# Kernel tuning notes

Hardware: AMD Instinct MI355X
Metric: run time of the kernel (lower is better)

The kernel has to match this reference:

```python
import jax, jax.numpy as jnp
import numpy as np

EMBED_DIM = 1024
NUM_HEADS = 16
HEAD_DIM = EMBED_DIM // NUM_HEADS


def setup_inputs() -> dict:
    key = jax.random.key(0)
    k_x, k_qkv, k_w, k_b = jax.random.split(key, 4)
    B, N, C = 2, 2048, EMBED_DIM
    scale = 1.0 / np.sqrt(C)
    x = jax.random.normal(k_x, (B, N, C), dtype=jnp.float32)
    # nn.Linear(embed_dim, 3*embed_dim, bias=False): weight [3C, C]
    w_qkv = jax.random.normal(k_qkv, (3 * C, C), dtype=jnp.float32) * scale
    # nn.Linear(embed_dim, embed_dim): weight [C, C], bias [C]
    w_out = jax.random.normal(k_w, (C, C), dtype=jnp.float32) * scale
    b_out = jax.random.normal(k_b, (C,), dtype=jnp.float32) * scale
    return {"x": x, "w_qkv": w_qkv, "w_out": w_out, "b_out": b_out}


def reference(x, w_qkv, w_out, b_out):
    B, N, C = x.shape
    H, D = NUM_HEADS, HEAD_DIM
    # qkv projection: [B,N,3C] -> [3,B,H,N,D]
    qkv = jnp.einsum("bnc,fc->bnf", x, w_qkv)
    qkv = qkv.reshape(B, N, 3, H, D).transpose(2, 0, 3, 1, 4)
    q, k, v = qkv[0], qkv[1], qkv[2]
    # scaled dot-product attention (dropout p=0 / eval mode -> identity)
    scores = jnp.einsum("bhnd,bhmd->bhnm", q, k) / np.sqrt(D).astype(x.dtype)
    attn = jax.nn.softmax(scores, axis=-1)
    out = jnp.einsum("bhnm,bhmd->bhnd", attn, v)
    out = out.transpose(0, 2, 1, 3).reshape(B, N, C)
    return jnp.einsum("bnc,oc->bno", out, w_out) + b_out
```

## Files before the change

### kernel.cpp

```cpp
#include <hip/hip_runtime.h>
#include <hip/hip_bf16.h>

typedef unsigned short u16;
typedef __attribute__((ext_vector_type(4))) float f32x4;
typedef __attribute__((ext_vector_type(8))) short bf16x8;

#define MFMA16(a, b, c) __builtin_amdgcn_mfma_f32_16x16x32_bf16(a, b, c, 0, 0, 0)

__device__ __forceinline__ u16 f2bf(float f) {
    union { float f; unsigned u; } v;
    v.f = f;
    unsigned r = v.u + 0x7FFFu + ((v.u >> 16) & 1u);
    return (u16)(r >> 16);
}

__device__ __forceinline__ float bf2f(u16 h) {
    union { unsigned u; float f; } v;
    v.u = ((unsigned)h) << 16;
    return v.f;
}

__device__ __forceinline__ int4 pack8(const float4 a, const float4 b) {
    int4 r;
    r.x = (int)((unsigned)f2bf(a.x) | ((unsigned)f2bf(a.y) << 16));
    r.y = (int)((unsigned)f2bf(a.z) | ((unsigned)f2bf(a.w) << 16));
    r.z = (int)((unsigned)f2bf(b.x) | ((unsigned)f2bf(b.y) << 16));
    r.w = (int)((unsigned)f2bf(b.z) | ((unsigned)f2bf(b.w) << 16));
    return r;
}

__device__ __forceinline__ unsigned pk2(float a, float b) {
    __hip_bfloat162 t = __float22bfloat162_rn(make_float2(a, b));
    union { __hip_bfloat162 h; unsigned u; } c;
    c.h = t;
    return c.u;
}

__device__ __forceinline__ bf16x8 mk_pa(f32x4 a, f32x4 b) {
    union { uint4 u; bf16x8 v; } r;
    r.u.x = pk2(a[0], a[1]);
    r.u.y = pk2(a[2], a[3]);
    r.u.z = pk2(b[0], b[1]);
    r.u.w = pk2(b[2], b[3]);
    return r.v;
}

__device__ __forceinline__ void gload_lds16(const u16* g, u16* l) {
    __builtin_amdgcn_global_load_lds(
        (const __attribute__((address_space(1))) void*)g,
        (__attribute__((address_space(3))) void*)l, 16, 0, 0);
}

__global__ __launch_bounds__(256) void cvt_kernel(
    const float* __restrict__ x, const float* __restrict__ wq,
    const float* __restrict__ wo, u16* __restrict__ outb)
{
    size_t i = ((size_t)blockIdx.x * 256 + threadIdx.x) * 8;
    const float* src;
    size_t off;
    if (i < 4194304)      { src = x;  off = i; }
    else if (i < 7340032) { src = wq; off = i - 4194304; }
    else                  { src = wo; off = i - 7340032; }
    float4 a = *(const float4*)(src + off);
    float4 b = *(const float4*)(src + off + 4);
    *(int4*)(outb + i) = pack8(a, b);
}

__global__ __launch_bounds__(512) void qkv_gemm_kernel(
    const u16* __restrict__ X, const u16* __restrict__ W,
    u16* __restrict__ qws, u16* __restrict__ kws, u16* __restrict__ vws)
{
    __shared__ __align__(16) u16 Ash[256 * 64];
    __shared__ __align__(16) u16 Bsh[128 * 64];
    const int id = blockIdx.x;
    const int xcd = id & 7, slot = id >> 3;
    const int bm = (xcd >> 1) * 4 + (slot & 3);
    const int bn = (xcd & 1) * 12 + (slot >> 2);
    const int tid = threadIdx.x;
    const int lane = tid & 63, wid = tid >> 6;
    const int wm = wid >> 1, wn = wid & 1;
    const int g = lane >> 4, lq = lane & 15;

    f32x4 acc[4][4];
#pragma unroll
    for (int i = 0; i < 4; i++)
#pragma unroll
        for (int j = 0; j < 4; j++) acc[i][j] = (f32x4){0.f, 0.f, 0.f, 0.f};

    const int lrow = lane >> 3;
    const int lchunk = (lane & 7) ^ lrow;
    const u16* Ab = X + (size_t)(bm * 256 + lrow) * 1024 + lchunk * 8;
    const u16* Bb = W + (size_t)(bn * 128 + lrow) * 1024 + lchunk * 8;

    for (int kt = 0; kt < 16; ++kt) {
#pragma unroll
        for (int i = 0; i < 4; i++) {
            int sub = wid * 4 + i;
            gload_lds16(Ab + (size_t)sub * 8192 + kt * 64, &Ash[sub * 512]);
        }
#pragma unroll
        for (int i = 0; i < 2; i++) {
            int sub = wid * 2 + i;
            gload_lds16(Bb + (size_t)sub * 8192 + kt * 64, &Bsh[sub * 512]);
        }
        __syncthreads();
#pragma unroll
        for (int ka = 0; ka < 2; ka++) {
            bf16x8 af[4], bfr[4];
#pragma unroll
            for (int mt = 0; mt < 4; mt++) {
                int row = wm * 64 + mt * 16 + lq;
                af[mt] = *(const bf16x8*)&Ash[row * 64 + (((ka * 4 + g) ^ (row & 7)) << 3)];
            }
#pragma unroll
            for (int nt = 0; nt < 4; nt++) {
                int row = wn * 64 + nt * 16 + lq;
                bfr[nt] = *(const bf16x8*)&Bsh[row * 64 + (((ka * 4 + g) ^ (row & 7)) << 3)];
            }
#pragma unroll
            for (int mt = 0; mt < 4; mt++)
#pragma unroll
                for (int nt = 0; nt < 4; nt++)
                    acc[mt][nt] = MFMA16(af[mt], bfr[nt], acc[mt][nt]);
        }
        __syncthreads();
    }

#pragma unroll
    for (int mt = 0; mt < 4; mt++) {
#pragma unroll
        for (int nt = 0; nt < 4; nt++) {
            int f = bn * 128 + wn * 64 + nt * 16 + lq;
            int t = f >> 10, h = (f >> 6) & 15, d = f & 63;
            int mbase = bm * 256 + wm * 64 + mt * 16 + g * 4;
            int b = mbase >> 11, n0 = mbase & 2047;
            if (t == 0) {
#pragma unroll
                for (int r = 0; r < 4; r++)
                    qws[((size_t)(b * 16 + h) * 2048 + n0 + r) * 64 + d] =
                        f2bf(acc[mt][nt][r] * 0.18033688f);
            } else if (t == 1) {
#pragma unroll
                for (int r = 0; r < 4; r++)
                    kws[((size_t)(b * 16 + h) * 2048 + n0 + r) * 64 + d] =
                        f2bf(acc[mt][nt][r]);
            } else {
                ushort4 pk;
                pk.x = f2bf(acc[mt][nt][0]);
                pk.y = f2bf(acc[mt][nt][1]);
                pk.z = f2bf(acc[mt][nt][2]);
                pk.w = f2bf(acc[mt][nt][3]);
                *(ushort4*)&vws[((size_t)(b * 16 + h) * 64 + d) * 2048 + n0] = pk;
            }
        }
    }
}

__global__ __launch_bounds__(256, 2) void attn_kernel(
    const u16* __restrict__ qws, const u16* __restrict__ kws,
    const u16* __restrict__ vws, u16* __restrict__ Opart,
    float* __restrict__ lpart)
{
    __shared__ __align__(16) u16 Ksh[2][64 * 64];
    __shared__ __align__(16) u16 Vsh[2][64 * 64];
    const int bh = blockIdx.x, qt = blockIdx.y, kvh = blockIdx.z;
    const int tid = threadIdx.x, wid = tid >> 6, lane = tid & 63;
    const int g = lane >> 4, lq = lane & 15;

    const u16* Qp = qws + ((size_t)bh * 2048 + qt * 128 + wid * 32) * 64;
    bf16x8 qf[2][2];
#pragma unroll
    for (int qa = 0; qa < 2; qa++) {
        qf[qa][0] = *(const bf16x8*)(Qp + (qa * 16 + lq) * 64 + g * 8);
        qf[qa][1] = *(const bf16x8*)(Qp + (qa * 16 + lq) * 64 + 32 + g * 8);
    }

    const int lr8 = lane >> 3;
    const int c0 = ((lane & 7) - lr8) & 7;
    const u16* Kb = kws + (size_t)bh * 2048 * 64;
    const u16* Vb = vws + (size_t)bh * 64 * 2048;

#define STAGE(TG, BUF)                                                        \
    {                                                                         \
        _Pragma("unroll")                                                     \
        for (int i = 0; i < 2; i++) {                                         \
            int sub = wid * 2 + i;                                            \
            int c = (c0 - 2 * sub) & 7;                                       \
            gload_lds16(Kb + (size_t)((TG) * 64 + sub * 8 + lr8) * 64 + c * 8,\
                        &Ksh[BUF][sub * 512]);                                \
            gload_lds16(Vb + (size_t)(sub * 8 + lr8) * 2048 + (TG) * 64 + c * 8,\
                        &Vsh[BUF][sub * 512]);                                \
        }                                                                     \
    }

    int koff[4][2];
#pragma unroll
    for (int j = 0; j < 4; j++) {
        int R = (j >> 1) * 32 + (lq >> 2) * 8 + (j & 1) * 4 + (lq & 3);
        koff[j][0] = R * 64 + (((g)     + (R & 7) + 2 * (R >> 3)) & 7) * 8;
        koff[j][1] = R * 64 + (((4 + g) + (R & 7) + 2 * (R >> 3)) & 7) * 8;
    }
    int voff[4][2];
#pragma unroll
    for (int dt = 0; dt < 4; dt++) {
        int vr = dt * 16 + lq;
        voff[dt][0] = vr * 64 + (((g)     + (vr & 7) + 2 * (vr >> 3)) & 7) * 8;
        voff[dt][1] = vr * 64 + (((4 + g) + (vr & 7) + 2 * (vr >> 3)) & 7) * 8;
    }

    bf16x8 onesB;
#pragma unroll
    for (int i = 0; i < 8; i++) onesB[i] = (short)0x3F80;

    f32x4 oacc[2][4];
#pragma unroll
    for (int qa = 0; qa < 2; qa++)
#pragma unroll
        for (int i = 0; i < 4; i++) oacc[qa][i] = (f32x4){0.f, 0.f, 0.f, 0.f};
    f32x4 lacc[2];
#pragma unroll
    for (int qa = 0; qa < 2; qa++) lacc[qa] = (f32x4){0.f, 0.f, 0.f, 0.f};

    const int tbase = kvh * 16;
    STAGE(tbase + 0, 0);

    for (int t = 0; t < 16; ++t) {
        const int buf = t & 1;
        asm volatile("s_waitcnt vmcnt(0)" ::: "memory");
        __builtin_amdgcn_s_barrier();
        __builtin_amdgcn_sched_barrier(0);
        if (t < 15) STAGE(tbase + t + 1, buf ^ 1);

        const u16* Kt = Ksh[buf];
        const u16* Vt = Vsh[buf];

        bf16x8 pa0[2], pa1[2];
        {
            f32x4 za[2], zb[2];
            bf16x8 k0 = *(const bf16x8*)&Kt[koff[0][0]];
            bf16x8 k1 = *(const bf16x8*)&Kt[koff[0][1]];
#pragma unroll
            for (int qa = 0; qa < 2; qa++) {
                f32x4 z = (f32x4){0.f, 0.f, 0.f, 0.f};
                z = MFMA16(k0, qf[qa][0], z);
                z = MFMA16(k1, qf[qa][1], z);
                za[qa] = z;
            }
            k0 = *(const bf16x8*)&Kt[koff[1][0]];
            k1 = *(const bf16x8*)&Kt[koff[1][1]];
#pragma unroll
            for (int qa = 0; qa < 2; qa++) {
                f32x4 z = (f32x4){0.f, 0.f, 0.f, 0.f};
                z = MFMA16(k0, qf[qa][0], z);
                z = MFMA16(k1, qf[qa][1], z);
                zb[qa] = z;
            }
#pragma unroll
            for (int qa = 0; qa < 2; qa++) {
#pragma unroll
                for (int r = 0; r < 4; r++) {
                    za[qa][r] = __builtin_amdgcn_exp2f(za[qa][r]);
                    zb[qa][r] = __builtin_amdgcn_exp2f(zb[qa][r]);
                }
                pa0[qa] = mk_pa(za[qa], zb[qa]);
            }
            k0 = *(const bf16x8*)&Kt[koff[2][0]];
            k1 = *(const bf16x8*)&Kt[koff[2][1]];
#pragma unroll
            for (int qa = 0; qa < 2; qa++) {
                f32x4 z = (f32x4){0.f, 0.f, 0.f, 0.f};
                z = MFMA16(k0, qf[qa][0], z);
                z = MFMA16(k1, qf[qa][1], z);
                za[qa] = z;
            }
            k0 = *(const bf16x8*)&Kt[koff[3][0]];
            k1 = *(const bf16x8*)&Kt[koff[3][1]];
#pragma unroll
            for (int qa = 0; qa < 2; qa++) {
                f32x4 z = (f32x4){0.f, 0.f, 0.f, 0.f};
                z = MFMA16(k0, qf[qa][0], z);
                z = MFMA16(k1, qf[qa][1], z);
                zb[qa] = z;
            }
#pragma unroll
            for (int qa = 0; qa < 2; qa++) {
#pragma unroll
                for (int r = 0; r < 4; r++) {
                    za[qa][r] = __builtin_amdgcn_exp2f(za[qa][r]);
                    zb[qa][r] = __builtin_amdgcn_exp2f(zb[qa][r]);
                }
                pa1[qa] = mk_pa(za[qa], zb[qa]);
            }
        }

        __builtin_amdgcn_s_setprio(1);
#pragma unroll
        for (int qa = 0; qa < 2; qa++) {
            lacc[qa] = MFMA16(pa0[qa], onesB, lacc[qa]);
            lacc[qa] = MFMA16(pa1[qa], onesB, lacc[qa]);
        }
#pragma unroll
        for (int dt = 0; dt < 4; dt++) {
            bf16x8 vb0 = *(const bf16x8*)&Vt[voff[dt][0]];
            bf16x8 vb1 = *(const bf16x8*)&Vt[voff[dt][1]];
#pragma unroll
            for (int qa = 0; qa < 2; qa++) {
                oacc[qa][dt] = MFMA16(pa0[qa], vb0, oacc[qa][dt]);
                oacc[qa][dt] = MFMA16(pa1[qa], vb1, oacc[qa][dt]);
            }
        }
        __builtin_amdgcn_s_setprio(0);
    }
#undef STAGE

    const int nbase = qt * 128 + wid * 32;
#pragma unroll
    for (int qa = 0; qa < 2; qa++) {
#pragma unroll
        for (int dt = 0; dt < 4; dt++)
#pragma unroll
            for (int r = 0; r < 4; r++) {
                int n = nbase + qa * 16 + g * 4 + r;
                Opart[(size_t)kvh * 4194304 + ((size_t)bh * 2048 + n) * 64 + dt * 16 + lq] =
                    f2bf(oacc[qa][dt][r]);
            }
        if (lq == 0) {
#pragma unroll
            for (int r = 0; r < 4; r++)
                lpart[kvh * 65536 + bh * 2048 + nbase + qa * 16 + g * 4 + r] =
                    lacc[qa][r];
        }
    }
}

__global__ __launch_bounds__(256) void combine_kernel(
    const u16* __restrict__ Opart, const float* __restrict__ lpart,
    u16* __restrict__ ows)
{
    int idx = blockIdx.x * 256 + threadIdx.x;
    int d4 = (idx & 15) * 4;
    int n  = (idx >> 4) & 2047;
    int bh = idx >> 15;
    size_t o = ((size_t)bh * 2048 + n) * 64 + d4;
    float s0 = 0.f, s1 = 0.f, s2 = 0.f, s3 = 0.f, l = 0.f;
#pragma unroll
    for (int s = 0; s < 2; s++) {
        ushort4 p = *(const ushort4*)(Opart + (size_t)s * 4194304 + o);
        s0 += bf2f(p.x);
        s1 += bf2f(p.y);
        s2 += bf2f(p.z);
        s3 += bf2f(p.w);
        l += lpart[s * 65536 + bh * 2048 + n];
    }
    float rl = 1.0f / l;
    ushort4 pk;
    pk.x = f2bf(s0 * rl);
    pk.y = f2bf(s1 * rl);
    pk.z = f2bf(s2 * rl);
    pk.w = f2bf(s3 * rl);
    int b = bh >> 4, h = bh & 15;
    *(ushort4*)&ows[((size_t)b * 2048 + n) * 1024 + h * 64 + d4] = pk;
}

__global__ __launch_bounds__(512) void out_gemm_kernel(
    const u16* __restrict__ A, const u16* __restrict__ W,
    const float* __restrict__ bias, float* __restrict__ Out)
{
    __shared__ __align__(16) u16 Ash[256 * 64];
    __shared__ __align__(16) u16 Bsh[128 * 64];
    const int id = blockIdx.x;
    const int xcd = id & 7, slot = id >> 3;
    const int bm = xcd * 2 + (slot & 1);
    const int bn = slot >> 1;
    const int tid = threadIdx.x;
    const int lane = tid & 63, wid = tid >> 6;
    const int wm = wid >> 1, wn = wid & 1;
    const int g = lane >> 4, lq = lane & 15;

    f32x4 acc[4][4];
#pragma unroll
    for (int i = 0; i < 4; i++)
#pragma unroll
        for (int j = 0; j < 4; j++) acc[i][j] = (f32x4){0.f, 0.f, 0.f, 0.f};

    const int lrow = lane >> 3;
    const int lchunk = (lane & 7) ^ lrow;
    const u16* Ab = A + (size_t)(bm * 256 + lrow) * 1024 + lchunk * 8;
    const u16* Bb = W + (size_t)(bn * 128 + lrow) * 1024 + lchunk * 8;

    for (int kt = 0; kt < 16; ++kt) {
#pragma unroll
        for (int i = 0; i < 4; i++) {
            int sub = wid * 4 + i;
            gload_lds16(Ab + (size_t)sub * 8192 + kt * 64, &Ash[sub * 512]);
        }
#pragma unroll
        for (int i = 0; i < 2; i++) {
            int sub = wid * 2 + i;
            gload_lds16(Bb + (size_t)sub * 8192 + kt * 64, &Bsh[sub * 512]);
        }
        __syncthreads();
#pragma unroll
        for (int ka = 0; ka < 2; ka++) {
            bf16x8 af[4], bfr[4];
#pragma unroll
            for (int mt = 0; mt < 4; mt++) {
                int row = wm * 64 + mt * 16 + lq;
                af[mt] = *(const bf16x8*)&Ash[row * 64 + (((ka * 4 + g) ^ (row & 7)) << 3)];
            }
#pragma unroll
            for (int nt = 0; nt < 4; nt++) {
                int row = wn * 64 + nt * 16 + lq;
                bfr[nt] = *(const bf16x8*)&Bsh[row * 64 + (((ka * 4 + g) ^ (row & 7)) << 3)];
            }
#pragma unroll
            for (int mt = 0; mt < 4; mt++)
#pragma unroll
                for (int nt = 0; nt < 4; nt++)
                    acc[mt][nt] = MFMA16(af[mt], bfr[nt], acc[mt][nt]);
        }
        __syncthreads();
    }

#pragma unroll
    for (int mt = 0; mt < 4; mt++) {
#pragma unroll
        for (int nt = 0; nt < 4; nt++) {
            int ncol = bn * 128 + wn * 64 + nt * 16 + lq;
            float bv = bias[ncol];
            int mbase = bm * 256 + wm * 64 + mt * 16 + g * 4;
#pragma unroll
            for (int r = 0; r < 4; r++)
                Out[(size_t)(mbase + r) * 1024 + ncol] = acc[mt][nt][r] + bv;
        }
    }
}

extern "C" void kernel_launch(void* const* d_in, const int* in_sizes, int n_in,
                              void* d_out, int out_size, void* d_ws, size_t ws_size,
                              hipStream_t stream) {
    const float* x     = (const float*)d_in[0];
    const float* w_qkv = (const float*)d_in[1];
    const float* w_out = (const float*)d_in[2];
    const float* b_out = (const float*)d_in[3];
    float* out = (float*)d_out;

    u16* xb  = (u16*)d_ws;
    u16* wqb = xb + 4194304;
    u16* wob = wqb + 3145728;
    u16* qws = wob + 1048576;
    u16* kws = qws + 4194304;
    u16* vws = kws + 4194304;
    u16* ows = vws + 4194304;
    u16* Opart = ows + 4194304;
    float* lpart = (float*)(Opart + 8388608);

    cvt_kernel<<<4096, 256, 0, stream>>>(x, w_qkv, w_out, xb);
    qkv_gemm_kernel<<<384, 512, 0, stream>>>(xb, wqb, qws, kws, vws);
    attn_kernel<<<dim3(32, 16, 2), 256, 0, stream>>>(qws, kws, vws, Opart, lpart);
    combine_kernel<<<4096, 256, 0, stream>>>(Opart, lpart, ows);
    out_gemm_kernel<<<128, 512, 0, stream>>>(ows, wob, b_out, out);
}
```

Baseline: 112.4 us.

## Double-buffer LDS tiles in QKV and output GEMMs to overlap loads with MFMA

Both projection GEMMs now keep two LDS buffers for the A and B tiles and issue global-to-LDS loads for the next k-step before computing on the current one. Each iteration waits on vmcnt and takes one barrier instead of two __syncthreads. The goal is to hide global load latency behind MFMA work. In exchange, LDS use per block doubles to 96 KB, which may limit occupancy, and the single barrier has to be enough to keep the buffer being overwritten safe from readers still using it.

```diff
diff --git a/kernel.cpp b/kernel.cpp
--- a/kernel.cpp
+++ b/kernel.cpp
@@ -70,8 +70,8 @@
     const u16* __restrict__ X, const u16* __restrict__ W,
     u16* __restrict__ qws, u16* __restrict__ kws, u16* __restrict__ vws)
 {
-    __shared__ __align__(16) u16 Ash[256 * 64];
-    __shared__ __align__(16) u16 Bsh[128 * 64];
+    __shared__ __align__(16) u16 Ash[2][256 * 64];
+    __shared__ __align__(16) u16 Bsh[2][128 * 64];
     const int id = blockIdx.x;
     const int xcd = id & 7, slot = id >> 3;
     const int bm = (xcd >> 1) * 4 + (slot & 3);
@@ -92,30 +92,43 @@
     const u16* Ab = X + (size_t)(bm * 256 + lrow) * 1024 + lchunk * 8;
     const u16* Bb = W + (size_t)(bn * 128 + lrow) * 1024 + lchunk * 8;
 
+#define QSTAGE(KT, BUF)                                                       \
+    {                                                                         \
+        _Pragma("unroll")                                                     \
+        for (int i = 0; i < 4; i++) {                                         \
+            int sub = wid * 4 + i;                                            \
+            gload_lds16(Ab + (size_t)sub * 8192 + (KT) * 64,                  \
+                        &Ash[BUF][sub * 512]);                                \
+        }                                                                     \
+        _Pragma("unroll")                                                     \
+        for (int i = 0; i < 2; i++) {                                         \
+            int sub = wid * 2 + i;                                            \
+            gload_lds16(Bb + (size_t)sub * 8192 + (KT) * 64,                  \
+                        &Bsh[BUF][sub * 512]);                                \
+        }                                                                     \
+    }
+
+    QSTAGE(0, 0);
+
     for (int kt = 0; kt < 16; ++kt) {
-#pragma unroll
-        for (int i = 0; i < 4; i++) {
-            int sub = wid * 4 + i;
-            gload_lds16(Ab + (size_t)sub * 8192 + kt * 64, &Ash[sub * 512]);
-        }
-#pragma unroll
-        for (int i = 0; i < 2; i++) {
-            int sub = wid * 2 + i;
-            gload_lds16(Bb + (size_t)sub * 8192 + kt * 64, &Bsh[sub * 512]);
-        }
-        __syncthreads();
+        const int buf = kt & 1;
+        asm volatile("s_waitcnt vmcnt(0)" ::: "memory");
+        __builtin_amdgcn_s_barrier();
+        __builtin_amdgcn_sched_barrier(0);
+        if (kt < 15) QSTAGE(kt + 1, buf ^ 1);
+
 #pragma unroll
         for (int ka = 0; ka < 2; ka++) {
             bf16x8 af[4], bfr[4];
 #pragma unroll
             for (int mt = 0; mt < 4; mt++) {
                 int row = wm * 64 + mt * 16 + lq;
-                af[mt] = *(const bf16x8*)&Ash[row * 64 + (((ka * 4 + g) ^ (row & 7)) << 3)];
+                af[mt] = *(const bf16x8*)&Ash[buf][row * 64 + (((ka * 4 + g) ^ (row & 7)) << 3)];
             }
 #pragma unroll
             for (int nt = 0; nt < 4; nt++) {
                 int row = wn * 64 + nt * 16 + lq;
-                bfr[nt] = *(const bf16x8*)&Bsh[row * 64 + (((ka * 4 + g) ^ (row & 7)) << 3)];
+                bfr[nt] = *(const bf16x8*)&Bsh[buf][row * 64 + (((ka * 4 + g) ^ (row & 7)) << 3)];
             }
 #pragma unroll
             for (int mt = 0; mt < 4; mt++)
@@ -123,8 +136,8 @@
                 for (int nt = 0; nt < 4; nt++)
                     acc[mt][nt] = MFMA16(af[mt], bfr[nt], acc[mt][nt]);
         }
-        __syncthreads();
-    }
+    }
+#undef QSTAGE
 
 #pragma unroll
     for (int mt = 0; mt < 4; mt++) {
@@ -366,8 +379,8 @@
     const u16* __restrict__ A, const u16* __restrict__ W,
     const float* __restrict__ bias, float* __restrict__ Out)
 {
-    __shared__ __align__(16) u16 Ash[256 * 64];
-    __shared__ __align__(16) u16 Bsh[128 * 64];
+    __shared__ __align__(16) u16 Ash[2][256 * 64];
+    __shared__ __align__(16) u16 Bsh[2][128 * 64];
     const int id = blockIdx.x;
     const int xcd = id & 7, slot = id >> 3;
     const int bm = xcd * 2 + (slot & 1);
@@ -388,30 +401,43 @@
     const u16* Ab = A + (size_t)(bm * 256 + lrow) * 1024 + lchunk * 8;
     const u16* Bb = W + (size_t)(bn * 128 + lrow) * 1024 + lchunk * 8;
 
+#define OSTAGE(KT, BUF)                                                       \
+    {                                                                         \
+        _Pragma("unroll")                                                     \
+        for (int i = 0; i < 4; i++) {                                         \
+            int sub = wid * 4 + i;                                            \
+            gload_lds16(Ab + (size_t)sub * 8192 + (KT) * 64,                  \
+                        &Ash[BUF][sub * 512]);                                \
+        }                                                                     \
+        _Pragma("unroll")                                                     \
+        for (int i = 0; i < 2; i++) {                                         \
+            int sub = wid * 2 + i;                                            \
+            gload_lds16(Bb + (size_t)sub * 8192 + (KT) * 64,                  \
+                        &Bsh[BUF][sub * 512]);                                \
+        }                                                                     \
+    }
+
+    OSTAGE(0, 0);
+
     for (int kt = 0; kt < 16; ++kt) {
-#pragma unroll
-        for (int i = 0; i < 4; i++) {
-            int sub = wid * 4 + i;
-            gload_lds16(Ab + (size_t)sub * 8192 + kt * 64, &Ash[sub * 512]);
-        }
-#pragma unroll
-        for (int i = 0; i < 2; i++) {
-            int sub = wid * 2 + i;
-            gload_lds16(Bb + (size_t)sub * 8192 + kt * 64, &Bsh[sub * 512]);
-        }
-        __syncthreads();
+        const int buf = kt & 1;
+        asm volatile("s_waitcnt vmcnt(0)" ::: "memory");
+        __builtin_amdgcn_s_barrier();
+        __builtin_amdgcn_sched_barrier(0);
+        if (kt < 15) OSTAGE(kt + 1, buf ^ 1);
+
 #pragma unroll
         for (int ka = 0; ka < 2; ka++) {
             bf16x8 af[4], bfr[4];
 #pragma unroll
             for (int mt = 0; mt < 4; mt++) {
                 int row = wm * 64 + mt * 16 + lq;
-                af[mt] = *(const bf16x8*)&Ash[row * 64 + (((ka * 4 + g) ^ (row & 7)) << 3)];
+                af[mt] = *(const bf16x8*)&Ash[buf][row * 64 + (((ka * 4 + g) ^ (row & 7)) << 3)];
             }
 #pragma unroll
             for (int nt = 0; nt < 4; nt++) {
                 int row = wn * 64 + nt * 16 + lq;
-                bfr[nt] = *(const bf16x8*)&Bsh[row * 64 + (((ka * 4 + g) ^ (row & 7)) << 3)];
+                bfr[nt] = *(const bf16x8*)&Bsh[buf][row * 64 + (((ka * 4 + g) ^ (row & 7)) << 3)];
             }
 #pragma unroll
             for (int mt = 0; mt < 4; mt++)
@@ -419,8 +445,8 @@
                 for (int nt = 0; nt < 4; nt++)
                     acc[mt][nt] = MFMA16(af[mt], bfr[nt], acc[mt][nt]);
         }
-        __syncthreads();
-    }
+    }
+#undef OSTAGE
 
 #pragma unroll
     for (int mt = 0; mt < 4; mt++) {
```

Result: slower. 129.6 us (+15.3%).
